# Kernel optimization log

Hardware: AMD Instinct MI355X
Metric: run time of the kernel (lower is better)

The kernel has to match this reference:

```python
import jax, jax.numpy as jnp
import numpy as np

STATE_DIM = 64
HIDDEN_DIM = 256
BATCH = 4096
DT = 0.01


def setup_inputs() -> dict:
    key = jax.random.key(0)
    ks = jax.random.split(key, 7)
    s = 1.0 / np.sqrt(STATE_DIM)
    h = 1.0 / np.sqrt(HIDDEN_DIM)
    return {
        "x0": jax.random.normal(ks[0], (BATCH, STATE_DIM), dtype=jnp.float32),
        "W1": jax.random.uniform(ks[1], (STATE_DIM, HIDDEN_DIM), jnp.float32, -s, s),
        "b1": jax.random.uniform(ks[2], (HIDDEN_DIM,), jnp.float32, -s, s),
        "W2": jax.random.uniform(ks[3], (HIDDEN_DIM, HIDDEN_DIM), jnp.float32, -h, h),
        "b2": jax.random.uniform(ks[4], (HIDDEN_DIM,), jnp.float32, -h, h),
        "W3": jax.random.uniform(ks[5], (HIDDEN_DIM, STATE_DIM), jnp.float32, -h, h),
        "b3": jax.random.uniform(ks[6], (STATE_DIM,), jnp.float32, -h, h),
        "dt_scale": jnp.ones((1,), dtype=jnp.float32) * 0.01,
        "steps": 200,
    }


def reference(x0, W1, b1, W2, b2, W3, b3, dt_scale, steps):
    def func(x):
        h1 = jnp.tanh(x @ W1 + b1)
        h2 = jnp.tanh(h1 @ W2 + b2)
        return h2 @ W3 + b3

    def step(x, _):
        x_next = x + func(x) * dt_scale * DT  # Euler update
        return x_next, x_next

    _, traj = jax.lax.scan(step, x0, None, length=steps)
    # traj: [steps, batch, state_dim] -> [batch, steps+1, state_dim]
    return jnp.concatenate([x0[:, None, :], jnp.swapaxes(traj, 0, 1)], axis=1)
```

## Files before the change

### kernel.cpp

```cpp
#include <hip/hip_runtime.h>


#define STATE_DIM 64
#define HIDDEN    256
#define TILE_M    16
#define NBLK      256
#define XPITCH    68
#define HPITCH    260

typedef short v8s __attribute__((ext_vector_type(8)));
typedef float v4f __attribute__((ext_vector_type(4)));

__device__ __forceinline__ unsigned short f2bf(float f) {
    return (unsigned short)((__float_as_uint(f) + 0x8000u) >> 16);
}
__device__ __forceinline__ unsigned pk2bf(float a, float b) {
    return ((__float_as_uint(a) + 0x8000u) >> 16) |
           ((__float_as_uint(b) + 0x8000u) & 0xffff0000u);
}
__device__ __forceinline__ float fast_tanh(float x) {
    float e = __builtin_amdgcn_exp2f(x * 2.8853900817779268f);
    return 1.0f - 2.0f * __builtin_amdgcn_rcpf(e + 1.0f);
}
__device__ __forceinline__ void sync_lds() {
    asm volatile("s_waitcnt lgkmcnt(0)" ::: "memory");
    __builtin_amdgcn_s_barrier();
    asm volatile("" ::: "memory");
}

__global__ void prep_weights(const float* __restrict__ W1,
                             const float* __restrict__ W2,
                             const float* __restrict__ W3,
                             short* __restrict__ W1t,
                             short* __restrict__ W2t,
                             short* __restrict__ W3t) {
    int u = blockIdx.x * 256 + threadIdx.x;
    if (u < 65536) {
        int n = u >> 8, k = u & 255;
        W2t[u] = (short)f2bf(W2[k * 256 + n]);
    }
    int v = u - 65536;
    if (v >= 0 && v < 16384) {
        int n = v >> 6, k = v & 63;
        W1t[v] = (short)f2bf(W1[k * 256 + n]);
    }
    int t = u - (65536 + 16384);
    if (t >= 0 && t < 16384) {
        int n = t >> 8, k = t & 255;
        W3t[t] = (short)f2bf(W3[k * 64 + n]);
    }
}

__global__ __launch_bounds__(512, 2)
void ode_kernel(const float* __restrict__ x0,
                const float* __restrict__ b1,
                const float* __restrict__ b2,
                const float* __restrict__ b3,
                const float* __restrict__ dt_scale,
                const int*   __restrict__ stepsp,
                const short* __restrict__ W1t,
                const short* __restrict__ W2t,
                const short* __restrict__ W3t,
                float* __restrict__ out) {
    __shared__ short xb [TILE_M * XPITCH];
    __shared__ short h1b[TILE_M * HPITCH];
    __shared__ short h2b[TILE_M * HPITCH];

    const int tid  = threadIdx.x;
    const int w    = tid >> 6;
    const int lane = tid & 63;
    const int ln   = lane & 15;
    const int q    = lane >> 4;
    const int blk  = blockIdx.x;
    const int nsteps = *stepsp;
    const float scale = dt_scale[0] * 0.01f;
    const int n0 = 32 * w;

    v8s w1f[2][2], w2f[2][8], w3f[8];
    #pragma unroll
    for (int t = 0; t < 2; t++)
        #pragma unroll
        for (int ks = 0; ks < 2; ks++)
            w1f[t][ks] = *(const v8s*)(W1t + (n0 + 16 * t + ln) * 64 + 32 * ks + 8 * q);
    #pragma unroll
    for (int t = 0; t < 2; t++)
        #pragma unroll
        for (int ks = 0; ks < 8; ks++)
            w2f[t][ks] = *(const v8s*)(W2t + (n0 + 16 * t + ln) * 256 + 32 * ks + 8 * q);
    if (w < 4) {
        #pragma unroll
        for (int ks = 0; ks < 8; ks++)
            w3f[ks] = *(const v8s*)(W3t + (16 * w + ln) * 256 + 32 * ks + 8 * q);
    }
    v4f b1v[2], b2v[2], b3v = {0.f, 0.f, 0.f, 0.f};
    #pragma unroll
    for (int t = 0; t < 2; t++) {
        b1v[t] = *(const v4f*)(b1 + n0 + 16 * t + 4 * q);
        b2v[t] = *(const v4f*)(b2 + n0 + 16 * t + 4 * q);
    }
    if (w < 4) b3v = *(const v4f*)(b3 + 16 * w + 4 * q);

    v4f x = {0.f, 0.f, 0.f, 0.f};
    unsigned tbase = 0;
    const int xw0 = ln * XPITCH + 16 * w + 4 * q;
    if (w < 4) {
        x = *(const v4f*)(x0 + (size_t)(blk * TILE_M + ln) * STATE_DIM + 16 * w + 4 * q);
        uint2 p; p.x = pk2bf(x[0], x[1]); p.y = pk2bf(x[2], x[3]);
        *(uint2*)(xb + xw0) = p;
        tbase = (unsigned)(blk * TILE_M + ln) * (unsigned)((nsteps + 1) * STATE_DIM)
              + 16 * w + 4 * q;
        *(v4f*)(out + tbase) = x;
        tbase += STATE_DIM;
    }
    __syncthreads();

    int xrd[2], hrd[8];
    #pragma unroll
    for (int ks = 0; ks < 2; ks++) xrd[ks] = ln * XPITCH + 32 * ks + 8 * q;
    #pragma unroll
    for (int ks = 0; ks < 8; ks++) hrd[ks] = ln * HPITCH + 32 * ks + 8 * q;
    const int hw0 = ln * HPITCH + n0 + 4 * q;

    for (int s = 0; s < nsteps; s++) {
        v8s xa0 = *(const v8s*)(xb + xrd[0]);
        v8s xa1 = *(const v8s*)(xb + xrd[1]);
        v4f a0 = b1v[0], a1 = b1v[1];
        a0 = __builtin_amdgcn_mfma_f32_16x16x32_bf16(w1f[0][0], xa0, a0, 0, 0, 0);
        a1 = __builtin_amdgcn_mfma_f32_16x16x32_bf16(w1f[1][0], xa0, a1, 0, 0, 0);
        a0 = __builtin_amdgcn_mfma_f32_16x16x32_bf16(w1f[0][1], xa1, a0, 0, 0, 0);
        a1 = __builtin_amdgcn_mfma_f32_16x16x32_bf16(w1f[1][1], xa1, a1, 0, 0, 0);
        {
            uint2 p0, p1;
            p0.x = pk2bf(fast_tanh(a0[0]), fast_tanh(a0[1]));
            p0.y = pk2bf(fast_tanh(a0[2]), fast_tanh(a0[3]));
            p1.x = pk2bf(fast_tanh(a1[0]), fast_tanh(a1[1]));
            p1.y = pk2bf(fast_tanh(a1[2]), fast_tanh(a1[3]));
            *(uint2*)(h1b + hw0)      = p0;
            *(uint2*)(h1b + hw0 + 16) = p1;
        }
        sync_lds();

        v8s ha[8];
        #pragma unroll
        for (int ks = 0; ks < 8; ks++) ha[ks] = *(const v8s*)(h1b + hrd[ks]);
        a0 = b2v[0]; a1 = b2v[1];
        #pragma unroll
        for (int ks = 0; ks < 8; ks++) {
            a0 = __builtin_amdgcn_mfma_f32_16x16x32_bf16(w2f[0][ks], ha[ks], a0, 0, 0, 0);
            a1 = __builtin_amdgcn_mfma_f32_16x16x32_bf16(w2f[1][ks], ha[ks], a1, 0, 0, 0);
        }
        {
            uint2 p0, p1;
            p0.x = pk2bf(fast_tanh(a0[0]), fast_tanh(a0[1]));
            p0.y = pk2bf(fast_tanh(a0[2]), fast_tanh(a0[3]));
            p1.x = pk2bf(fast_tanh(a1[0]), fast_tanh(a1[1]));
            p1.y = pk2bf(fast_tanh(a1[2]), fast_tanh(a1[3]));
            *(uint2*)(h2b + hw0)      = p0;
            *(uint2*)(h2b + hw0 + 16) = p1;
        }
        sync_lds();

        if (w < 4) {
            v8s hc[8];
            #pragma unroll
            for (int ks = 0; ks < 8; ks++) hc[ks] = *(const v8s*)(h2b + hrd[ks]);
            v4f a3 = b3v;
            #pragma unroll
            for (int ks = 0; ks < 8; ks++)
                a3 = __builtin_amdgcn_mfma_f32_16x16x32_bf16(w3f[ks], hc[ks], a3, 0, 0, 0);
            #pragma unroll
            for (int i = 0; i < 4; i++)
                x[i] = fmaf(a3[i], scale, x[i]);
            uint2 p; p.x = pk2bf(x[0], x[1]); p.y = pk2bf(x[2], x[3]);
            *(uint2*)(xb + xw0) = p;
            *(v4f*)(out + tbase) = x;
            tbase += STATE_DIM;
        }
        sync_lds();
    }
}

extern "C" void kernel_launch(void* const* d_in, const int* in_sizes, int n_in,
                              void* d_out, int out_size, void* d_ws, size_t ws_size,
                              hipStream_t stream) {
    const float* x0 = (const float*)d_in[0];
    const float* W1 = (const float*)d_in[1];
    const float* b1 = (const float*)d_in[2];
    const float* W2 = (const float*)d_in[3];
    const float* b2 = (const float*)d_in[4];
    const float* W3 = (const float*)d_in[5];
    const float* b3 = (const float*)d_in[6];
    const float* dt = (const float*)d_in[7];
    const int* steps = (const int*)d_in[8];

    short* W1t = (short*)d_ws;
    short* W2t = W1t + 64 * 256;
    short* W3t = W2t + 256 * 256;

    prep_weights<<<384, 256, 0, stream>>>(W1, W2, W3, W1t, W2t, W3t);
    ode_kernel<<<NBLK, 512, 0, stream>>>(x0, b1, b2, b3, dt, steps,
                                         W1t, W2t, W3t, (float*)d_out);
}
```

Before: 433.1 us.

## Halve waves per block so each wave computes 64 hidden columns

Cuts the block from 8 waves to 4. Each wave now owns 64 hidden columns (4 MFMA tiles) in layers 1 and 2, and every wave takes part in layer 3, so no waves sit idle in that stage. Layer 3 is split into two independent accumulator chains to shorten its MFMA dependency chain. The goal is cheaper barriers, more independent MFMAs per wave and no idle waves. The cost is higher register pressure from holding twice the weight fragments, and fewer waves to hide latency.

```diff
diff --git a/kernel.cpp b/kernel.cpp
--- a/kernel.cpp
+++ b/kernel.cpp
@@ -51,7 +51,7 @@
     }
 }
 
-__global__ __launch_bounds__(512, 2)
+__global__ __launch_bounds__(256, 1)
 void ode_kernel(const float* __restrict__ x0,
                 const float* __restrict__ b1,
                 const float* __restrict__ b2,
@@ -74,44 +74,43 @@
     const int blk  = blockIdx.x;
     const int nsteps = *stepsp;
     const float scale = dt_scale[0] * 0.01f;
-    const int n0 = 32 * w;
-
-    v8s w1f[2][2], w2f[2][8], w3f[8];
-    #pragma unroll
-    for (int t = 0; t < 2; t++)
+    const int n0 = 64 * w;
+    const int m0 = 16 * w;
+
+    v8s w1f[4][2], w2f[4][8], w3f[8];
+    #pragma unroll
+    for (int t = 0; t < 4; t++)
         #pragma unroll
         for (int ks = 0; ks < 2; ks++)
             w1f[t][ks] = *(const v8s*)(W1t + (n0 + 16 * t + ln) * 64 + 32 * ks + 8 * q);
     #pragma unroll
-    for (int t = 0; t < 2; t++)
+    for (int t = 0; t < 4; t++)
         #pragma unroll
         for (int ks = 0; ks < 8; ks++)
             w2f[t][ks] = *(const v8s*)(W2t + (n0 + 16 * t + ln) * 256 + 32 * ks + 8 * q);
-    if (w < 4) {
-        #pragma unroll
-        for (int ks = 0; ks < 8; ks++)
-            w3f[ks] = *(const v8s*)(W3t + (16 * w + ln) * 256 + 32 * ks + 8 * q);
-    }
-    v4f b1v[2], b2v[2], b3v = {0.f, 0.f, 0.f, 0.f};
-    #pragma unroll
-    for (int t = 0; t < 2; t++) {
+    #pragma unroll
+    for (int ks = 0; ks < 8; ks++)
+        w3f[ks] = *(const v8s*)(W3t + (m0 + ln) * 256 + 32 * ks + 8 * q);
+
+    v4f b1v[4], b2v[4], b3v;
+    #pragma unroll
+    for (int t = 0; t < 4; t++) {
         b1v[t] = *(const v4f*)(b1 + n0 + 16 * t + 4 * q);
         b2v[t] = *(const v4f*)(b2 + n0 + 16 * t + 4 * q);
     }
-    if (w < 4) b3v = *(const v4f*)(b3 + 16 * w + 4 * q);
-
-    v4f x = {0.f, 0.f, 0.f, 0.f};
-    unsigned tbase = 0;
-    const int xw0 = ln * XPITCH + 16 * w + 4 * q;
-    if (w < 4) {
-        x = *(const v4f*)(x0 + (size_t)(blk * TILE_M + ln) * STATE_DIM + 16 * w + 4 * q);
+    b3v = *(const v4f*)(b3 + m0 + 4 * q);
+
+    v4f x;
+    const int xw0 = ln * XPITCH + m0 + 4 * q;
+    x = *(const v4f*)(x0 + (size_t)(blk * TILE_M + ln) * STATE_DIM + m0 + 4 * q);
+    {
         uint2 p; p.x = pk2bf(x[0], x[1]); p.y = pk2bf(x[2], x[3]);
         *(uint2*)(xb + xw0) = p;
-        tbase = (unsigned)(blk * TILE_M + ln) * (unsigned)((nsteps + 1) * STATE_DIM)
-              + 16 * w + 4 * q;
-        *(v4f*)(out + tbase) = x;
-        tbase += STATE_DIM;
-    }
+    }
+    unsigned tbase = (unsigned)(blk * TILE_M + ln) * (unsigned)((nsteps + 1) * STATE_DIM)
+                   + m0 + 4 * q;
+    *(v4f*)(out + tbase) = x;
+    tbase += STATE_DIM;
     __syncthreads();
 
     int xrd[2], hrd[8];
@@ -124,53 +123,55 @@
     for (int s = 0; s < nsteps; s++) {
         v8s xa0 = *(const v8s*)(xb + xrd[0]);
         v8s xa1 = *(const v8s*)(xb + xrd[1]);
-        v4f a0 = b1v[0], a1 = b1v[1];
-        a0 = __builtin_amdgcn_mfma_f32_16x16x32_bf16(w1f[0][0], xa0, a0, 0, 0, 0);
-        a1 = __builtin_amdgcn_mfma_f32_16x16x32_bf16(w1f[1][0], xa0, a1, 0, 0, 0);
-        a0 = __builtin_amdgcn_mfma_f32_16x16x32_bf16(w1f[0][1], xa1, a0, 0, 0, 0);
-        a1 = __builtin_amdgcn_mfma_f32_16x16x32_bf16(w1f[1][1], xa1, a1, 0, 0, 0);
+        v4f a[4];
+        #pragma unroll
+        for (int t = 0; t < 4; t++) {
+            a[t] = b1v[t];
+            a[t] = __builtin_amdgcn_mfma_f32_16x16x32_bf16(w1f[t][0], xa0, a[t], 0, 0, 0);
+            a[t] = __builtin_amdgcn_mfma_f32_16x16x32_bf16(w1f[t][1], xa1, a[t], 0, 0, 0);
+        }
+        #pragma unroll
+        for (int t = 0; t < 4; t++) {
+            uint2 p;
+            p.x = pk2bf(fast_tanh(a[t][0]), fast_tanh(a[t][1]));
+            p.y = pk2bf(fast_tanh(a[t][2]), fast_tanh(a[t][3]));
+            *(uint2*)(h1b + hw0 + 16 * t) = p;
+        }
+        sync_lds();
+
+        v8s ha[8];
+        #pragma unroll
+        for (int ks = 0; ks < 8; ks++) ha[ks] = *(const v8s*)(h1b + hrd[ks]);
+        #pragma unroll
+        for (int t = 0; t < 4; t++) a[t] = b2v[t];
+        #pragma unroll
+        for (int ks = 0; ks < 8; ks++)
+            #pragma unroll
+            for (int t = 0; t < 4; t++)
+                a[t] = __builtin_amdgcn_mfma_f32_16x16x32_bf16(w2f[t][ks], ha[ks], a[t], 0, 0, 0);
+        #pragma unroll
+        for (int t = 0; t < 4; t++) {
+            uint2 p;
+            p.x = pk2bf(fast_tanh(a[t][0]), fast_tanh(a[t][1]));
+            p.y = pk2bf(fast_tanh(a[t][2]), fast_tanh(a[t][3]));
+            *(uint2*)(h2b + hw0 + 16 * t) = p;
+        }
+        sync_lds();
+
         {
-            uint2 p0, p1;
-            p0.x = pk2bf(fast_tanh(a0[0]), fast_tanh(a0[1]));
-            p0.y = pk2bf(fast_tanh(a0[2]), fast_tanh(a0[3]));
-            p1.x = pk2bf(fast_tanh(a1[0]), fast_tanh(a1[1]));
-            p1.y = pk2bf(fast_tanh(a1[2]), fast_tanh(a1[3]));
-            *(uint2*)(h1b + hw0)      = p0;
-            *(uint2*)(h1b + hw0 + 16) = p1;
-        }
-        sync_lds();
-
-        v8s ha[8];
-        #pragma unroll
-        for (int ks = 0; ks < 8; ks++) ha[ks] = *(const v8s*)(h1b + hrd[ks]);
-        a0 = b2v[0]; a1 = b2v[1];
-        #pragma unroll
-        for (int ks = 0; ks < 8; ks++) {
-            a0 = __builtin_amdgcn_mfma_f32_16x16x32_bf16(w2f[0][ks], ha[ks], a0, 0, 0, 0);
-            a1 = __builtin_amdgcn_mfma_f32_16x16x32_bf16(w2f[1][ks], ha[ks], a1, 0, 0, 0);
-        }
-        {
-            uint2 p0, p1;
-            p0.x = pk2bf(fast_tanh(a0[0]), fast_tanh(a0[1]));
-            p0.y = pk2bf(fast_tanh(a0[2]), fast_tanh(a0[3]));
-            p1.x = pk2bf(fast_tanh(a1[0]), fast_tanh(a1[1]));
-            p1.y = pk2bf(fast_tanh(a1[2]), fast_tanh(a1[3]));
-            *(uint2*)(h2b + hw0)      = p0;
-            *(uint2*)(h2b + hw0 + 16) = p1;
-        }
-        sync_lds();
-
-        if (w < 4) {
             v8s hc[8];
             #pragma unroll
             for (int ks = 0; ks < 8; ks++) hc[ks] = *(const v8s*)(h2b + hrd[ks]);
             v4f a3 = b3v;
-            #pragma unroll
-            for (int ks = 0; ks < 8; ks++)
-                a3 = __builtin_amdgcn_mfma_f32_16x16x32_bf16(w3f[ks], hc[ks], a3, 0, 0, 0);
+            v4f c3 = {0.f, 0.f, 0.f, 0.f};
+            #pragma unroll
+            for (int ks = 0; ks < 4; ks++) {
+                a3 = __builtin_amdgcn_mfma_f32_16x16x32_bf16(w3f[ks],     hc[ks],     a3, 0, 0, 0);
+                c3 = __builtin_amdgcn_mfma_f32_16x16x32_bf16(w3f[ks + 4], hc[ks + 4], c3, 0, 0, 0);
+            }
             #pragma unroll
             for (int i = 0; i < 4; i++)
-                x[i] = fmaf(a3[i], scale, x[i]);
+                x[i] = fmaf(a3[i] + c3[i], scale, x[i]);
             uint2 p; p.x = pk2bf(x[0], x[1]); p.y = pk2bf(x[2], x[3]);
             *(uint2*)(xb + xw0) = p;
             *(v4f*)(out + tbase) = x;
@@ -198,6 +199,6 @@
     short* W3t = W2t + 256 * 256;
 
     prep_weights<<<384, 256, 0, stream>>>(W1, W2, W3, W1t, W2t, W3t);
-    ode_kernel<<<NBLK, 512, 0, stream>>>(x0, b1, b2, b3, dt, steps,
+    ode_kernel<<<NBLK, 256, 0, stream>>>(x0, b1, b2, b3, dt, steps,
                                          W1t, W2t, W3t, (float*)d_out);
 }
```

Result: slower. 521.5 us (+20.4%).
